# Kernel optimization log

Measured on AMD Instinct MI355X. Metric: run time of the kernel, lower is better.

## Reference

```python
import jax, jax.numpy as jnp
import numpy as np

B, T, C = 2, 2048, 768
NH = 12
HS = C // NH


def setup_inputs() -> dict:
    key = jax.random.key(0)
    k1, k2, k3 = jax.random.split(key, 3)
    x = jax.random.normal(k1, (B, T, C), dtype=jnp.float32)
    # c_attn: Linear(C, 3C). Stored as (C, 3C) so y = x @ w + b (same math as torch x @ W.T + b).
    w_attn = jax.random.normal(k2, (C, 3 * C), dtype=jnp.float32) * (1.0 / np.sqrt(C))
    b_attn = jax.random.normal(k3, (3 * C,), dtype=jnp.float32) * 0.02
    return {"x": x, "w_attn": w_attn, "b_attn": b_attn}


def reference(x, w_attn, b_attn):
    b, t, c = x.shape
    qkv = x @ w_attn + b_attn                      # [B, T, 3C]
    q, k, v = jnp.split(qkv, 3, axis=-1)
    # [B, T, C] -> [B, NH, T, HS]
    q = q.reshape(b, t, NH, HS).transpose(0, 2, 1, 3)
    k = k.reshape(b, t, NH, HS).transpose(0, 2, 1, 3)
    v = v.reshape(b, t, NH, HS).transpose(0, 2, 1, 3)
    scale = 1.0 / np.sqrt(HS).astype(np.float32)
    wei = jnp.einsum("bhqd,bhkd->bhqk", q, k) * scale   # [B, NH, T, T]
    causal = jnp.tril(jnp.ones((t, t), dtype=bool))
    wei = jnp.where(causal[None, None, :, :], wei, -jnp.inf)
    wei = jax.nn.softmax(wei, axis=-1)
    out = jnp.einsum("bhqk,bhkd->bhqd", wei, v)          # [B, NH, T, HS]
    # NOTE: original module returns here, before head-merge / output projection.
    return out
```

## Files before the change

kernel.cpp:

```cpp
#include <hip/hip_runtime.h>

typedef __bf16 bf16_t;
typedef __bf16 bf16x8 __attribute__((ext_vector_type(8)));
typedef __bf16 bf16x4 __attribute__((ext_vector_type(4)));
typedef _Float16 f16x2 __attribute__((ext_vector_type(2)));
typedef _Float16 f16x4 __attribute__((ext_vector_type(4)));
typedef _Float16 f16x8 __attribute__((ext_vector_type(8)));
typedef float f32x4 __attribute__((ext_vector_type(4)));

#define B_   2
#define T_   2048
#define C_   768
#define NH_  12
#define HS_  64
#define N3_  2304
#define M_   4096
#define QSCALE 0.18033688011112042f

__device__ __forceinline__ bf16_t f2bf(float f) {
  unsigned u = __builtin_bit_cast(unsigned, f);
  u += 0x7fffu + ((u >> 16) & 1u);
  unsigned short s = (unsigned short)(u >> 16);
  return __builtin_bit_cast(bf16_t, s);
}

__global__ __launch_bounds__(256) void cvt_xw_kernel(const float* __restrict__ x,
                                                     const float* __restrict__ w,
                                                     bf16_t* __restrict__ xb,
                                                     bf16_t* __restrict__ wt) {
  __shared__ float tile[32][33];
  int bx = blockIdx.x;
  if (bx < 3072) {
    int i = (bx * 256 + threadIdx.x) * 4;
    float4 v = *reinterpret_cast<const float4*>(x + i);
    xb[i + 0] = f2bf(v.x);
    xb[i + 1] = f2bf(v.y);
    xb[i + 2] = f2bf(v.z);
    xb[i + 3] = f2bf(v.w);
  } else {
    int b = bx - 3072;
    int k0 = (b % 24) * 32, n0 = (b / 24) * 32;
    int tx = threadIdx.x & 31, ty = threadIdx.x >> 5;
#pragma unroll
    for (int i = 0; i < 4; i++)
      tile[ty + i * 8][tx] = w[(size_t)(k0 + ty + i * 8) * N3_ + n0 + tx];
    __syncthreads();
#pragma unroll
    for (int i = 0; i < 4; i++)
      wt[(size_t)(n0 + ty + i * 8) * C_ + k0 + tx] = f2bf(tile[tx][ty + i * 8]);
  }
}

__global__ __launch_bounds__(256) void gemm_qkv(const bf16_t* __restrict__ xb,
                                                const bf16_t* __restrict__ wt,
                                                const float* __restrict__ bias,
                                                bf16_t* __restrict__ qout,
                                                bf16_t* __restrict__ kout,
                                                _Float16* __restrict__ va) {
  __shared__ bf16_t As[2][64 * 32];
  __shared__ bf16_t Bs[2][128 * 32];
  const int tid = threadIdx.x;
  const int lane = tid & 63, wave = tid >> 6;
  const int wm = wave >> 1, wn = wave & 1;
  const int quad = lane >> 4, l15 = lane & 15;

  const int id = (int)blockIdx.x;
  const int xcd = id & 7, r = id >> 3;
  const int cx = r % 9, ry = r / 9;
  const int bx = (xcd & 1) * 9 + cx;
  const int by = (xcd >> 1) * 16 + ry;
  const int row0 = by * 64;
  const int col0 = bx * 128;
  const bool isqk = (col0 < 1536);

  f32x4 acc[2][4];
#pragma unroll
  for (int mi = 0; mi < 2; mi++)
#pragma unroll
    for (int ni = 0; ni < 4; ni++) acc[mi][ni] = f32x4{0.f, 0.f, 0.f, 0.f};

  const int r0 = tid >> 2, q0 = tid & 3;
  const int r1 = (256 + tid) >> 2, q1 = (256 + tid) & 3;
  const bf16_t* gA0 = xb + (size_t)(row0 + r0) * C_ + q0 * 8;
  const bf16_t* gB0 = wt + (size_t)(col0 + r0) * C_ + q0 * 8;
  const bf16_t* gB1 = wt + (size_t)(col0 + r1) * C_ + q1 * 8;
  const int ldsOff0 = (wave * 64) * 16;
  const int ldsOff1 = (256 + wave * 64) * 16;

  auto STAGE = [&](int buf, int k0) {
    __builtin_amdgcn_global_load_lds((const __attribute__((address_space(1))) void*)(gA0 + k0),
                                     (__attribute__((address_space(3))) void*)((char*)As[buf] + ldsOff0), 16, 0, 0);
    __builtin_amdgcn_global_load_lds((const __attribute__((address_space(1))) void*)(gB0 + k0),
                                     (__attribute__((address_space(3))) void*)((char*)Bs[buf] + ldsOff0), 16, 0, 0);
    __builtin_amdgcn_global_load_lds((const __attribute__((address_space(1))) void*)(gB1 + k0),
                                     (__attribute__((address_space(3))) void*)((char*)Bs[buf] + ldsOff1), 16, 0, 0);
  };

  STAGE(0, 0);
  __syncthreads();

  constexpr int NT = C_ / 32;
#pragma unroll 2
  for (int t = 0; t < NT; ++t) {
    const int cur = t & 1;
    if (t + 1 < NT) STAGE(cur ^ 1, (t + 1) * 32);

    bf16x8 af[2], bfr[4];
#pragma unroll
    for (int mi = 0; mi < 2; mi++)
      af[mi] = *reinterpret_cast<const bf16x8*>(&As[cur][(wm * 32 + mi * 16 + l15) * 32 + quad * 8]);
#pragma unroll
    for (int ni = 0; ni < 4; ni++)
      bfr[ni] = *reinterpret_cast<const bf16x8*>(&Bs[cur][(wn * 64 + ni * 16 + l15) * 32 + quad * 8]);
    if (isqk) {
#pragma unroll
      for (int mi = 0; mi < 2; mi++)
#pragma unroll
        for (int ni = 0; ni < 4; ni++)
          acc[mi][ni] = __builtin_amdgcn_mfma_f32_16x16x32_bf16(bfr[ni], af[mi], acc[mi][ni], 0, 0, 0);
    } else {
#pragma unroll
      for (int mi = 0; mi < 2; mi++)
#pragma unroll
        for (int ni = 0; ni < 4; ni++)
          acc[mi][ni] = __builtin_amdgcn_mfma_f32_16x16x32_bf16(af[mi], bfr[ni], acc[mi][ni], 0, 0, 0);
    }
    __syncthreads();
  }

  if (isqk) {
#pragma unroll
    for (int mi = 0; mi < 2; mi++) {
      int t = row0 + wm * 32 + mi * 16 + l15;
      int b = t >> 11, tt = t & 2047;
#pragma unroll
      for (int ni = 0; ni < 4; ni++) {
        int cN0 = col0 + wn * 64 + ni * 16 + quad * 4;
        int which = cN0 / 768;
        int rem = cN0 - which * 768;
        int h = rem >> 6, d0 = rem & 63;
        float4 bv = *reinterpret_cast<const float4*>(bias + cN0);
        float sc = which ? 1.0f : QSCALE;
        bf16x4 pack;
        pack[0] = f2bf((acc[mi][ni][0] + bv.x) * sc);
        pack[1] = f2bf((acc[mi][ni][1] + bv.y) * sc);
        pack[2] = f2bf((acc[mi][ni][2] + bv.z) * sc);
        pack[3] = f2bf((acc[mi][ni][3] + bv.w) * sc);
        bf16_t* dst = which ? kout : qout;
        *reinterpret_cast<bf16x4*>(dst + (((size_t)b * NH_ + h) * T_ + tt) * HS_ + d0) = pack;
      }
    }
  } else {
#pragma unroll
    for (int mi = 0; mi < 2; mi++) {
      int trow = row0 + wm * 32 + mi * 16 + quad * 4;
      int b = trow >> 11, tt = trow & 2047;
      int kt = tt >> 6, nj = (tt >> 4) & 3, qd = (tt >> 2) & 3;
#pragma unroll
      for (int ni = 0; ni < 4; ni++) {
        int cN = col0 + wn * 64 + ni * 16 + l15;
        int rem = cN - 1536;
        int h = rem >> 6, d = rem & 63;
        int bh = b * NH_ + h;
        float bv = bias[cN];
        f16x4 pk;
#pragma unroll
        for (int r2 = 0; r2 < 4; r2++) pk[r2] = (_Float16)(acc[mi][ni][r2] + bv);
        size_t off = ((((((size_t)bh * 32 + kt) * 4 + nj) * 4 + qd) * 16 + (d & 15)) * 16) + (d >> 4) * 4;
        *reinterpret_cast<f16x4*>(va + off) = pk;
      }
    }
  }
}

__global__ __launch_bounds__(128) void attn_kernel(const bf16_t* __restrict__ qb,
                                                   const bf16_t* __restrict__ kb,
                                                   const _Float16* __restrict__ va,
                                                   float* __restrict__ out) {
  __shared__ bf16_t Ks[2][64][72];
  __shared__ _Float16 Vs[2][4][2][64][8];
  const int tid = threadIdx.x;
  const int lane = tid & 63, wave = tid >> 6;
  const int quad = lane >> 4, l15 = lane & 15;
  const int id = (int)blockIdx.x;
  const int xcd = id & 7, within = id >> 3;
  const int bh = xcd * 3 + within / 32;
  const int pairIdx = within & 31;
  const bf16_t* Qg = qb + (size_t)bh * T_ * HS_;
  const bf16_t* Kg = kb + (size_t)bh * T_ * HS_;
  const _Float16* Vg = va + (size_t)bh * 32 * 4096;

  const int krow = tid >> 1, kcolB = (tid & 1) * 64;
  const int vni = tid >> 5, vlane = (tid & 31) * 2;

  int4 rk0, rk1, rk2, rk3, rv0, rv1, rv2, rv3;
  const char* kp;
  const char* vp;
  auto GLOAD = [&]() {
    rk0 = *reinterpret_cast<const int4*>(kp);
    rk1 = *reinterpret_cast<const int4*>(kp + 16);
    rk2 = *reinterpret_cast<const int4*>(kp + 32);
    rk3 = *reinterpret_cast<const int4*>(kp + 48);
    rv0 = *reinterpret_cast<const int4*>(vp);
    rv1 = *reinterpret_cast<const int4*>(vp + 16);
    rv2 = *reinterpret_cast<const int4*>(vp + 32);
    rv3 = *reinterpret_cast<const int4*>(vp + 48);
    kp += 8192; vp += 8192;
  };
  auto SSTORE = [&](int buf) {
    char* kd = (char*)&Ks[buf][krow][0] + kcolB;
    *reinterpret_cast<int4*>(kd) = rk0;
    *reinterpret_cast<int4*>(kd + 16) = rk1;
    *reinterpret_cast<int4*>(kd + 32) = rk2;
    *reinterpret_cast<int4*>(kd + 48) = rk3;
    *reinterpret_cast<int4*>(&Vs[buf][vni][0][vlane][0]) = rv0;
    *reinterpret_cast<int4*>(&Vs[buf][vni][1][vlane][0]) = rv1;
    *reinterpret_cast<int4*>(&Vs[buf][vni][0][vlane + 1][0]) = rv2;
    *reinterpret_cast<int4*>(&Vs[buf][vni][1][vlane + 1][0]) = rv3;
  };

#pragma unroll
  for (int part = 0; part < 2; part++) {
    const int qtile = part ? pairIdx : 63 - pairIdx;
    const int qrow_base = qtile * 32 + wave * 16;
    const int qmax = qrow_base + 15;
    const int qcol = qrow_base + l15;
    const int nkt = (qtile >> 1) + 1;

    bf16x8 bq0 = *reinterpret_cast<const bf16x8*>(Qg + (size_t)qcol * HS_ + quad * 8);
    bf16x8 bq1 = *reinterpret_cast<const bf16x8*>(Qg + (size_t)qcol * HS_ + 32 + quad * 8);

    float lsum = 0.f;
    f32x4 Oacc[4];
#pragma unroll
    for (int mi = 0; mi < 4; mi++) Oacc[mi] = f32x4{0.f, 0.f, 0.f, 0.f};

    kp = (const char*)Kg + krow * 128 + kcolB;
    vp = (const char*)Vg + tid * 64;
    GLOAD();
    __syncthreads();
    SSTORE(0);
    __syncthreads();

    for (int kt = 0; kt < nkt; kt++) {
      const int cur = kt & 1;
      const bool last = (kt + 1 >= nkt);
      if (!last) GLOAD();

      const bool diag = (kt == nkt - 1);
      f16x4 pf[4];
#pragma unroll
      for (int ni = 0; ni < 4; ni++) {
        if (diag && (kt * 64 + ni * 16 > qmax)) continue;
        bf16x8 ka0 = *reinterpret_cast<const bf16x8*>(&Ks[cur][ni * 16 + l15][quad * 8]);
        bf16x8 ka1 = *reinterpret_cast<const bf16x8*>(&Ks[cur][ni * 16 + l15][32 + quad * 8]);
        f32x4 s = {0.f, 0.f, 0.f, 0.f};
        s = __builtin_amdgcn_mfma_f32_16x16x32_bf16(ka0, bq0, s, 0, 0, 0);
        s = __builtin_amdgcn_mfma_f32_16x16x32_bf16(ka1, bq1, s, 0, 0, 0);
        float p0 = __builtin_amdgcn_exp2f(s[0]);
        float p1 = __builtin_amdgcn_exp2f(s[1]);
        float p2 = __builtin_amdgcn_exp2f(s[2]);
        float p3 = __builtin_amdgcn_exp2f(s[3]);
        if (diag) {
          int jb = kt * 64 + ni * 16 + quad * 4;
          if (jb + 0 > qcol) p0 = 0.f;
          if (jb + 1 > qcol) p1 = 0.f;
          if (jb + 2 > qcol) p2 = 0.f;
          if (jb + 3 > qcol) p3 = 0.f;
        }
        lsum += (p0 + p1) + (p2 + p3);
        f16x2 lo2 = __builtin_bit_cast(f16x2, __builtin_amdgcn_cvt_pkrtz(p0, p1));
        f16x2 hi2 = __builtin_bit_cast(f16x2, __builtin_amdgcn_cvt_pkrtz(p2, p3));
        pf[ni] = f16x4{lo2[0], lo2[1], hi2[0], hi2[1]};
      }
#pragma unroll
      for (int ni = 0; ni < 4; ni++) {
        if (diag && (kt * 64 + ni * 16 > qmax)) continue;
#pragma unroll
        for (int p = 0; p < 2; p++) {
          f16x8 vv = *reinterpret_cast<const f16x8*>(&Vs[cur][ni][p][lane][0]);
          f16x4 lo = __builtin_shufflevector(vv, vv, 0, 1, 2, 3);
          f16x4 hi = __builtin_shufflevector(vv, vv, 4, 5, 6, 7);
          Oacc[2 * p]     = __builtin_amdgcn_mfma_f32_16x16x16f16(lo, pf[ni], Oacc[2 * p], 0, 0, 0);
          Oacc[2 * p + 1] = __builtin_amdgcn_mfma_f32_16x16x16f16(hi, pf[ni], Oacc[2 * p + 1], 0, 0, 0);
        }
      }

      if (!last) {
        SSTORE(1 - cur);
        __syncthreads();
      }
    }

    lsum += __shfl_xor(lsum, 16, 64);
    lsum += __shfl_xor(lsum, 32, 64);
    float rinv = 1.0f / lsum;

#pragma unroll
    for (int mi = 0; mi < 4; mi++) {
      float4 o;
      o.x = Oacc[mi][0] * rinv;
      o.y = Oacc[mi][1] * rinv;
      o.z = Oacc[mi][2] * rinv;
      o.w = Oacc[mi][3] * rinv;
      *reinterpret_cast<float4*>(out + ((size_t)bh * T_ + qcol) * HS_ + mi * 16 + quad * 4) = o;
    }
  }
}

extern "C" void kernel_launch(void* const* d_in, const int* in_sizes, int n_in,
                              void* d_out, int out_size, void* d_ws, size_t ws_size,
                              hipStream_t stream) {
  const float* x = (const float*)d_in[0];
  const float* w = (const float*)d_in[1];
  const float* bias = (const float*)d_in[2];
  float* out = (float*)d_out;

  char* ws = (char*)d_ws;
  bf16_t* xb = (bf16_t*)(ws);
  bf16_t* wt = (bf16_t*)(ws + 6291456);
  bf16_t* qb = (bf16_t*)(ws + 6291456 + 3538944);
  bf16_t* kb = qb + 3145728;
  _Float16* va = (_Float16*)(kb + 3145728);

  cvt_xw_kernel<<<dim3(3072 + 1728), dim3(256), 0, stream>>>(x, w, xb, wt);
  gemm_qkv<<<dim3(1152), dim3(256), 0, stream>>>(xb, wt, bias, qb, kb, va);
  attn_kernel<<<dim3(768), dim3(128), 0, stream>>>(qb, kb, va, out);
}
```

Before: 141.1 us.

## Process 64-row query tiles per block, reusing K/V fragments across two row groups

Replaces the paired 32-row query tiles per block with a single 64-row tile, where each wave computes two 16-row groups sharing the same K/V LDS reads. This halves K/V global loads and LDS traffic per query row and drops the second pass's prologue. Blocks are ordered largest tile first, but per-block work is no longer balanced, and register pressure roughly doubles for accumulators.

```diff
diff --git a/kernel.cpp b/kernel.cpp
--- a/kernel.cpp
+++ b/kernel.cpp
@@ -183,9 +183,9 @@
   const int lane = tid & 63, wave = tid >> 6;
   const int quad = lane >> 4, l15 = lane & 15;
   const int id = (int)blockIdx.x;
-  const int xcd = id & 7, within = id >> 3;
-  const int bh = xcd * 3 + within / 32;
-  const int pairIdx = within & 31;
+  const int xcd = id & 7, r = id >> 3;
+  const int bh = xcd * 3 + (r % 3);
+  const int qtile = 31 - r / 3;
   const bf16_t* Qg = qb + (size_t)bh * T_ * HS_;
   const bf16_t* Kg = kb + (size_t)bh * T_ * HS_;
   const _Float16* Vg = va + (size_t)bh * 32 * 4096;
@@ -219,92 +219,126 @@
     *reinterpret_cast<int4*>(&Vs[buf][vni][1][vlane + 1][0]) = rv3;
   };
 
-#pragma unroll
-  for (int part = 0; part < 2; part++) {
-    const int qtile = part ? pairIdx : 63 - pairIdx;
-    const int qrow_base = qtile * 32 + wave * 16;
-    const int qmax = qrow_base + 15;
-    const int qcol = qrow_base + l15;
-    const int nkt = (qtile >> 1) + 1;
-
-    bf16x8 bq0 = *reinterpret_cast<const bf16x8*>(Qg + (size_t)qcol * HS_ + quad * 8);
-    bf16x8 bq1 = *reinterpret_cast<const bf16x8*>(Qg + (size_t)qcol * HS_ + 32 + quad * 8);
-
-    float lsum = 0.f;
-    f32x4 Oacc[4];
-#pragma unroll
-    for (int mi = 0; mi < 4; mi++) Oacc[mi] = f32x4{0.f, 0.f, 0.f, 0.f};
-
-    kp = (const char*)Kg + krow * 128 + kcolB;
-    vp = (const char*)Vg + tid * 64;
-    GLOAD();
-    __syncthreads();
-    SSTORE(0);
-    __syncthreads();
-
-    for (int kt = 0; kt < nkt; kt++) {
-      const int cur = kt & 1;
-      const bool last = (kt + 1 >= nkt);
-      if (!last) GLOAD();
-
-      const bool diag = (kt == nkt - 1);
-      f16x4 pf[4];
-#pragma unroll
-      for (int ni = 0; ni < 4; ni++) {
-        if (diag && (kt * 64 + ni * 16 > qmax)) continue;
-        bf16x8 ka0 = *reinterpret_cast<const bf16x8*>(&Ks[cur][ni * 16 + l15][quad * 8]);
-        bf16x8 ka1 = *reinterpret_cast<const bf16x8*>(&Ks[cur][ni * 16 + l15][32 + quad * 8]);
+  const int qrow_base = qtile * 64 + wave * 32;
+  const int qmax = qrow_base + 31;
+  const int qcol0 = qrow_base + l15;
+  const int qcol1 = qrow_base + 16 + l15;
+  const int nkt = qtile + 1;
+
+  bf16x8 bq00 = *reinterpret_cast<const bf16x8*>(Qg + (size_t)qcol0 * HS_ + quad * 8);
+  bf16x8 bq01 = *reinterpret_cast<const bf16x8*>(Qg + (size_t)qcol0 * HS_ + 32 + quad * 8);
+  bf16x8 bq10 = *reinterpret_cast<const bf16x8*>(Qg + (size_t)qcol1 * HS_ + quad * 8);
+  bf16x8 bq11 = *reinterpret_cast<const bf16x8*>(Qg + (size_t)qcol1 * HS_ + 32 + quad * 8);
+
+  float lsum0 = 0.f, lsum1 = 0.f;
+  f32x4 Oa[4], Ob[4];
+#pragma unroll
+  for (int mi = 0; mi < 4; mi++) { Oa[mi] = f32x4{0.f, 0.f, 0.f, 0.f}; Ob[mi] = f32x4{0.f, 0.f, 0.f, 0.f}; }
+
+  kp = (const char*)Kg + krow * 128 + kcolB;
+  vp = (const char*)Vg + tid * 64;
+  GLOAD();
+  SSTORE(0);
+  __syncthreads();
+
+  for (int kt = 0; kt < nkt; kt++) {
+    const int cur = kt & 1;
+    const bool last = (kt + 1 >= nkt);
+    if (!last) GLOAD();
+
+    const bool diag = (kt == nkt - 1);
+    f16x4 pf0[4], pf1[4];
+#pragma unroll
+    for (int ni = 0; ni < 4; ni++) {
+      if (diag && (kt * 64 + ni * 16 > qmax)) continue;
+      bf16x8 ka0 = *reinterpret_cast<const bf16x8*>(&Ks[cur][ni * 16 + l15][quad * 8]);
+      bf16x8 ka1 = *reinterpret_cast<const bf16x8*>(&Ks[cur][ni * 16 + l15][32 + quad * 8]);
+      {
         f32x4 s = {0.f, 0.f, 0.f, 0.f};
-        s = __builtin_amdgcn_mfma_f32_16x16x32_bf16(ka0, bq0, s, 0, 0, 0);
-        s = __builtin_amdgcn_mfma_f32_16x16x32_bf16(ka1, bq1, s, 0, 0, 0);
+        s = __builtin_amdgcn_mfma_f32_16x16x32_bf16(ka0, bq00, s, 0, 0, 0);
+        s = __builtin_amdgcn_mfma_f32_16x16x32_bf16(ka1, bq01, s, 0, 0, 0);
         float p0 = __builtin_amdgcn_exp2f(s[0]);
         float p1 = __builtin_amdgcn_exp2f(s[1]);
         float p2 = __builtin_amdgcn_exp2f(s[2]);
         float p3 = __builtin_amdgcn_exp2f(s[3]);
         if (diag) {
           int jb = kt * 64 + ni * 16 + quad * 4;
-          if (jb + 0 > qcol) p0 = 0.f;
-          if (jb + 1 > qcol) p1 = 0.f;
-          if (jb + 2 > qcol) p2 = 0.f;
-          if (jb + 3 > qcol) p3 = 0.f;
+          if (jb + 0 > qcol0) p0 = 0.f;
+          if (jb + 1 > qcol0) p1 = 0.f;
+          if (jb + 2 > qcol0) p2 = 0.f;
+          if (jb + 3 > qcol0) p3 = 0.f;
         }
-        lsum += (p0 + p1) + (p2 + p3);
+        lsum0 += (p0 + p1) + (p2 + p3);
         f16x2 lo2 = __builtin_bit_cast(f16x2, __builtin_amdgcn_cvt_pkrtz(p0, p1));
         f16x2 hi2 = __builtin_bit_cast(f16x2, __builtin_amdgcn_cvt_pkrtz(p2, p3));
-        pf[ni] = f16x4{lo2[0], lo2[1], hi2[0], hi2[1]};
-      }
-#pragma unroll
-      for (int ni = 0; ni < 4; ni++) {
-        if (diag && (kt * 64 + ni * 16 > qmax)) continue;
-#pragma unroll
-        for (int p = 0; p < 2; p++) {
-          f16x8 vv = *reinterpret_cast<const f16x8*>(&Vs[cur][ni][p][lane][0]);
-          f16x4 lo = __builtin_shufflevector(vv, vv, 0, 1, 2, 3);
-          f16x4 hi = __builtin_shufflevector(vv, vv, 4, 5, 6, 7);
-          Oacc[2 * p]     = __builtin_amdgcn_mfma_f32_16x16x16f16(lo, pf[ni], Oacc[2 * p], 0, 0, 0);
-          Oacc[2 * p + 1] = __builtin_amdgcn_mfma_f32_16x16x16f16(hi, pf[ni], Oacc[2 * p + 1], 0, 0, 0);
+        pf0[ni] = f16x4{lo2[0], lo2[1], hi2[0], hi2[1]};
+      }
+      {
+        f32x4 s = {0.f, 0.f, 0.f, 0.f};
+        s = __builtin_amdgcn_mfma_f32_16x16x32_bf16(ka0, bq10, s, 0, 0, 0);
+        s = __builtin_amdgcn_mfma_f32_16x16x32_bf16(ka1, bq11, s, 0, 0, 0);
+        float p0 = __builtin_amdgcn_exp2f(s[0]);
+        float p1 = __builtin_amdgcn_exp2f(s[1]);
+        float p2 = __builtin_amdgcn_exp2f(s[2]);
+        float p3 = __builtin_amdgcn_exp2f(s[3]);
+        if (diag) {
+          int jb = kt * 64 + ni * 16 + quad * 4;
+          if (jb + 0 > qcol1) p0 = 0.f;
+          if (jb + 1 > qcol1) p1 = 0.f;
+          if (jb + 2 > qcol1) p2 = 0.f;
+          if (jb + 3 > qcol1) p3 = 0.f;
         }
-      }
-
-      if (!last) {
-        SSTORE(1 - cur);
-        __syncthreads();
-      }
-    }
-
-    lsum += __shfl_xor(lsum, 16, 64);
-    lsum += __shfl_xor(lsum, 32, 64);
-    float rinv = 1.0f / lsum;
-
-#pragma unroll
-    for (int mi = 0; mi < 4; mi++) {
-      float4 o;
-      o.x = Oacc[mi][0] * rinv;
-      o.y = Oacc[mi][1] * rinv;
-      o.z = Oacc[mi][2] * rinv;
-      o.w = Oacc[mi][3] * rinv;
-      *reinterpret_cast<float4*>(out + ((size_t)bh * T_ + qcol) * HS_ + mi * 16 + quad * 4) = o;
-    }
+        lsum1 += (p0 + p1) + (p2 + p3);
+        f16x2 lo2 = __builtin_bit_cast(f16x2, __builtin_amdgcn_cvt_pkrtz(p0, p1));
+        f16x2 hi2 = __builtin_bit_cast(f16x2, __builtin_amdgcn_cvt_pkrtz(p2, p3));
+        pf1[ni] = f16x4{lo2[0], lo2[1], hi2[0], hi2[1]};
+      }
+    }
+#pragma unroll
+    for (int ni = 0; ni < 4; ni++) {
+      if (diag && (kt * 64 + ni * 16 > qmax)) continue;
+#pragma unroll
+      for (int p = 0; p < 2; p++) {
+        f16x8 vv = *reinterpret_cast<const f16x8*>(&Vs[cur][ni][p][lane][0]);
+        f16x4 lo = __builtin_shufflevector(vv, vv, 0, 1, 2, 3);
+        f16x4 hi = __builtin_shufflevector(vv, vv, 4, 5, 6, 7);
+        Oa[2 * p]     = __builtin_amdgcn_mfma_f32_16x16x16f16(lo, pf0[ni], Oa[2 * p], 0, 0, 0);
+        Oa[2 * p + 1] = __builtin_amdgcn_mfma_f32_16x16x16f16(hi, pf0[ni], Oa[2 * p + 1], 0, 0, 0);
+        Ob[2 * p]     = __builtin_amdgcn_mfma_f32_16x16x16f16(lo, pf1[ni], Ob[2 * p], 0, 0, 0);
+        Ob[2 * p + 1] = __builtin_amdgcn_mfma_f32_16x16x16f16(hi, pf1[ni], Ob[2 * p + 1], 0, 0, 0);
+      }
+    }
+
+    if (!last) {
+      SSTORE(1 - cur);
+      __syncthreads();
+    }
+  }
+
+  lsum0 += __shfl_xor(lsum0, 16, 64);
+  lsum0 += __shfl_xor(lsum0, 32, 64);
+  lsum1 += __shfl_xor(lsum1, 16, 64);
+  lsum1 += __shfl_xor(lsum1, 32, 64);
+  float rinv0 = 1.0f / lsum0;
+  float rinv1 = 1.0f / lsum1;
+
+#pragma unroll
+  for (int mi = 0; mi < 4; mi++) {
+    float4 o;
+    o.x = Oa[mi][0] * rinv0;
+    o.y = Oa[mi][1] * rinv0;
+    o.z = Oa[mi][2] * rinv0;
+    o.w = Oa[mi][3] * rinv0;
+    *reinterpret_cast<float4*>(out + ((size_t)bh * T_ + qcol0) * HS_ + mi * 16 + quad * 4) = o;
+  }
+#pragma unroll
+  for (int mi = 0; mi < 4; mi++) {
+    float4 o;
+    o.x = Ob[mi][0] * rinv1;
+    o.y = Ob[mi][1] * rinv1;
+    o.z = Ob[mi][2] * rinv1;
+    o.w = Ob[mi][3] * rinv1;
+    *reinterpret_cast<float4*>(out + ((size_t)bh * T_ + qcol1) * HS_ + mi * 16 + quad * 4) = o;
   }
 }
 
```

After: 174.0 us. 23.3% more time.

## Load V fragments directly from global into registers, bypassing LDS

Applied to the files above, without the earlier changes.

The QKV projection epilogue now writes V in a layout where each lane's MFMA operand is a contiguous 16-byte chunk per (ni, p). The attention kernel drops the shared-memory V buffer and reads V straight from global memory into registers at the start of each key tile. This removes the LDS stores and reads for V and halves shared-memory use, but it puts global load latency on the critical path within the iteration (there is no prefetch one tile ahead) and both waves load the same V data redundantly.

```diff
diff --git a/kernel.cpp b/kernel.cpp
--- a/kernel.cpp
+++ b/kernel.cpp
@@ -166,7 +166,9 @@
         f16x4 pk;
 #pragma unroll
         for (int r2 = 0; r2 < 4; r2++) pk[r2] = (_Float16)(acc[mi][ni][r2] + bv);
-        size_t off = ((((((size_t)bh * 32 + kt) * 4 + nj) * 4 + qd) * 16 + (d & 15)) * 16) + (d >> 4) * 4;
+        size_t off = (size_t)bh * 131072 + (size_t)kt * 4096 + (size_t)nj * 1024
+                   + (size_t)((d >> 5) & 1) * 512 + (size_t)qd * 128
+                   + (size_t)(d & 15) * 8 + (size_t)((d >> 4) & 1) * 4;
         *reinterpret_cast<f16x4*>(va + off) = pk;
       }
     }
@@ -178,7 +180,6 @@
                                                    const _Float16* __restrict__ va,
                                                    float* __restrict__ out) {
   __shared__ bf16_t Ks[2][64][72];
-  __shared__ _Float16 Vs[2][4][2][64][8];
   const int tid = threadIdx.x;
   const int lane = tid & 63, wave = tid >> 6;
   const int quad = lane >> 4, l15 = lane & 15;
@@ -188,24 +189,18 @@
   const int pairIdx = within & 31;
   const bf16_t* Qg = qb + (size_t)bh * T_ * HS_;
   const bf16_t* Kg = kb + (size_t)bh * T_ * HS_;
-  const _Float16* Vg = va + (size_t)bh * 32 * 4096;
+  const _Float16* Vg = va + (size_t)bh * 131072;
 
   const int krow = tid >> 1, kcolB = (tid & 1) * 64;
-  const int vni = tid >> 5, vlane = (tid & 31) * 2;
-
-  int4 rk0, rk1, rk2, rk3, rv0, rv1, rv2, rv3;
+
+  int4 rk0, rk1, rk2, rk3;
   const char* kp;
-  const char* vp;
   auto GLOAD = [&]() {
     rk0 = *reinterpret_cast<const int4*>(kp);
     rk1 = *reinterpret_cast<const int4*>(kp + 16);
     rk2 = *reinterpret_cast<const int4*>(kp + 32);
     rk3 = *reinterpret_cast<const int4*>(kp + 48);
-    rv0 = *reinterpret_cast<const int4*>(vp);
-    rv1 = *reinterpret_cast<const int4*>(vp + 16);
-    rv2 = *reinterpret_cast<const int4*>(vp + 32);
-    rv3 = *reinterpret_cast<const int4*>(vp + 48);
-    kp += 8192; vp += 8192;
+    kp += 8192;
   };
   auto SSTORE = [&](int buf) {
     char* kd = (char*)&Ks[buf][krow][0] + kcolB;
@@ -213,10 +208,6 @@
     *reinterpret_cast<int4*>(kd + 16) = rk1;
     *reinterpret_cast<int4*>(kd + 32) = rk2;
     *reinterpret_cast<int4*>(kd + 48) = rk3;
-    *reinterpret_cast<int4*>(&Vs[buf][vni][0][vlane][0]) = rv0;
-    *reinterpret_cast<int4*>(&Vs[buf][vni][1][vlane][0]) = rv1;
-    *reinterpret_cast<int4*>(&Vs[buf][vni][0][vlane + 1][0]) = rv2;
-    *reinterpret_cast<int4*>(&Vs[buf][vni][1][vlane + 1][0]) = rv3;
   };
 
 #pragma unroll
@@ -236,7 +227,6 @@
     for (int mi = 0; mi < 4; mi++) Oacc[mi] = f32x4{0.f, 0.f, 0.f, 0.f};
 
     kp = (const char*)Kg + krow * 128 + kcolB;
-    vp = (const char*)Vg + tid * 64;
     GLOAD();
     __syncthreads();
     SSTORE(0);
@@ -246,6 +236,14 @@
       const int cur = kt & 1;
       const bool last = (kt + 1 >= nkt);
       if (!last) GLOAD();
+
+      const _Float16* Vt = Vg + (size_t)kt * 4096 + lane * 8;
+      f16x8 vR[4][2];
+#pragma unroll
+      for (int ni = 0; ni < 4; ni++) {
+        vR[ni][0] = *reinterpret_cast<const f16x8*>(Vt + ni * 1024);
+        vR[ni][1] = *reinterpret_cast<const f16x8*>(Vt + ni * 1024 + 512);
+      }
 
       const bool diag = (kt == nkt - 1);
       f16x4 pf[4];
@@ -278,7 +276,7 @@
         if (diag && (kt * 64 + ni * 16 > qmax)) continue;
 #pragma unroll
         for (int p = 0; p < 2; p++) {
-          f16x8 vv = *reinterpret_cast<const f16x8*>(&Vs[cur][ni][p][lane][0]);
+          f16x8 vv = vR[ni][p];
           f16x4 lo = __builtin_shufflevector(vv, vv, 0, 1, 2, 3);
           f16x4 hi = __builtin_shufflevector(vv, vv, 4, 5, 6, 7);
           Oacc[2 * p]     = __builtin_amdgcn_mfma_f32_16x16x16f16(lo, pf[ni], Oacc[2 * p], 0, 0, 0);
```

Measured after the change: 145.6 us. 1.03x slower.
